# Performance work log

Measured on AMD Instinct MI355X. Metric: run time of the kernel, lower is better.

Reference implementation:

```python
import jax, jax.numpy as jnp
import numpy as np

NUM_ITERATIONS = 5
NUM_TERMS = 3  # (degree + 1) // 2 with degree = 5
INITIAL_SCALE = 1.1


def setup_inputs() -> dict:
    key = jax.random.key(0)
    k1, k2 = jax.random.split(key)
    X = jax.random.normal(k1, (64, 1024, 1024), dtype=jnp.float32)
    coefficients = jnp.array([3.4445, -4.7750, 2.0315], dtype=jnp.float32)
    return {"X": X, "coefficients": coefficients}


def reference(X, coefficients):
    # Normalize each matrix to Frobenius norm INITIAL_SCALE
    fro = jnp.sqrt(jnp.sum(X * X, axis=(-2, -1), keepdims=True))
    X = X / fro * INITIAL_SCALE
    for _ in range(NUM_ITERATIONS):
        # XTX = X^T X, shape [B, M, M]
        XTX = jnp.einsum('bji,bjk->bik', X, X)
        term = X
        acc = coefficients[0] * X
        for i in range(1, NUM_TERMS):
            term = jnp.einsum('bij,bjk->bik', term, XTX)  # X (X^T X)^i
            acc = acc + coefficients[i] * term
        X = acc
    return X
```

## Files before the change

kernel.cpp:

```cpp
#include <hip/hip_runtime.h>
#include <hip/hip_bf16.h>
#include <stdint.h>

typedef float f32x4 __attribute__((ext_vector_type(4)));
typedef short bf16x8 __attribute__((ext_vector_type(8)));

#define LDW 1024
#define BATCH_SH 20

__device__ __forceinline__ float b2f(__hip_bfloat16 h) { return __bfloat162float(h); }
__device__ __forceinline__ __hip_bfloat16 f2b(float f) { return __float2bfloat16(f); }

__device__ __forceinline__ void gload16(const void* g, void* l) {
  __builtin_amdgcn_global_load_lds((const __attribute__((address_space(1))) void*)g,
                                   (__attribute__((address_space(3))) void*)l,
                                   16, 0, 0);
}

__global__ void k_partial(const float* __restrict__ xin, float* __restrict__ partials) {
  const int b = blockIdx.y, ch = blockIdx.x, t = threadIdx.x;
  const size_t base = ((size_t)b << BATCH_SH) + (size_t)ch * 16384;
  float s = 0.f;
#pragma unroll
  for (int i = 0; i < 16; ++i) {
    f32x4 v = *reinterpret_cast<const f32x4*>(xin + base + (size_t)(i * 256 + t) * 4);
    s += v[0] * v[0] + v[1] * v[1] + v[2] * v[2] + v[3] * v[3];
  }
#pragma unroll
  for (int off = 32; off; off >>= 1) s += __shfl_down(s, off);
  __shared__ float red[4];
  if ((t & 63) == 0) red[t >> 6] = s;
  __syncthreads();
  if (t == 0) partials[b * 64 + ch] = red[0] + red[1] + red[2] + red[3];
}

__global__ void k_scalesplit(const float* __restrict__ xin, const float* __restrict__ partials,
                             __hip_bfloat16* __restrict__ Xh, __hip_bfloat16* __restrict__ Xl,
                             __hip_bfloat16* __restrict__ XTh, __hip_bfloat16* __restrict__ XTl) {
  __shared__ float tile[64][65];
  const int b = blockIdx.z, tm = blockIdx.y, tn = blockIdx.x;
  const size_t boff = (size_t)b << BATCH_SH;
  const int t = threadIdx.x, lr0 = t >> 6, lc = t & 63;
  float q = partials[b * 64 + (t & 63)];
#pragma unroll
  for (int off = 32; off; off >>= 1) q += __shfl_down(q, off);
  q = __shfl(q, 0);
  const float s = 1.1f / sqrtf(q);
#pragma unroll
  for (int p = 0; p < 16; ++p) {
    const int lr = p * 4 + lr0;
    const size_t idx = boff + (size_t)(tm * 64 + lr) * LDW + tn * 64 + lc;
    const float v = xin[idx] * s;
    __hip_bfloat16 h = f2b(v);
    Xh[idx] = h;
    Xl[idx] = f2b(v - b2f(h));
    tile[lr][lc] = v;
  }
  __syncthreads();
#pragma unroll
  for (int p = 0; p < 16; ++p) {
    const int lr = p * 4 + lr0;
    const float v = tile[lc][lr];
    const size_t idx = boff + (size_t)(tn * 64 + lr) * LDW + tm * 64 + lc;
    __hip_bfloat16 h = f2b(v);
    XTh[idx] = h;
    XTl[idx] = f2b(v - b2f(h));
  }
}


#define SEGPTRS(S)                                                                        \
  const int seg_ = (S) >> 4, k0_ = ((S) & 15) << 6;                                       \
  const __hip_bfloat16* pa_ = seg_ == 0 ? pa0 : seg_ == 1 ? pa1 : pa2;                    \
  const __hip_bfloat16* pb_ = seg_ == 0 ? pb0 : seg_ == 1 ? pb1 : pb2;

#define STAGE_GL(DB, S)                                                                   \
  {                                                                                       \
    SEGPTRS(S)                                                                            \
    char* lb_ = smem + (DB) * 65536;                                                      \
    _Pragma("unroll") for (int it_ = 0; it_ < 4; ++it_) {                                 \
      const int r_ = it_ * 64 + w * 8 + (l >> 3);                                         \
      const int kx_ = k0_ + (((l & 7) ^ (l >> 3)) << 3);                                  \
      gload16(pa_ + boff + (size_t)(rowA + r_) * LDW + kx_,                               \
              lb_ + (it_ * 64 + w * 8) * 128 + l * 16);                                   \
      gload16(pb_ + boff + (size_t)(rowB + r_) * LDW + kx_,                               \
              lb_ + 32768 + (it_ * 64 + w * 8) * 128 + l * 16);                           \
    }                                                                                     \
  }

#define MFMA_CL(AV, BV)                                                                   \
  __builtin_amdgcn_s_setprio(1);                                                          \
  _Pragma("unroll") for (int mi_ = 0; mi_ < 8; ++mi_)                                     \
      _Pragma("unroll") for (int ni_ = 0; ni_ < 4; ++ni_)                                 \
          acc[mi_][ni_] = __builtin_amdgcn_mfma_f32_16x16x32_bf16(                        \
              AV[mi_], BV[ni_], acc[mi_][ni_], 0, 0, 0);                                  \
  __builtin_amdgcn_s_setprio(0);

#define SCB() __builtin_amdgcn_sched_barrier(0)
#define BAR() __builtin_amdgcn_s_barrier()

template <int MODE>
__global__ __launch_bounds__(512, 2) void k_gemm(
    const __hip_bfloat16* __restrict__ pa0, const __hip_bfloat16* __restrict__ pa1,
    const __hip_bfloat16* __restrict__ pa2, const __hip_bfloat16* __restrict__ pb0,
    const __hip_bfloat16* __restrict__ pb1, const __hip_bfloat16* __restrict__ pb2,
    __hip_bfloat16* oh, __hip_bfloat16* ol,
    __hip_bfloat16* oth, __hip_bfloat16* otl,
    float* __restrict__ of,
    const __hip_bfloat16* __restrict__ eh, const __hip_bfloat16* __restrict__ el,
    const float* __restrict__ coef) {
  __shared__ __align__(16) char smem[131072];
  const int t = threadIdx.x;
  const int w = t >> 6, l = t & 63;
  const int wr = w >> 2, wc = w & 3;

  const int nwg = gridDim.x, q = nwg >> 3, r8 = nwg & 7;
  const int xcd = blockIdx.x & 7, o = blockIdx.x >> 3;
  const int wgid = (xcd < r8 ? xcd * (q + 1) : r8 * (q + 1) + (xcd - r8) * q) + o;

  int bat, tm, tn;
  if constexpr (MODE == 3) {
    bat = wgid >> 4;
    const int tile = wgid & 15;
    tm = tile >> 2; tn = tile & 3;
  } else {
    bat = (int)((unsigned)wgid / 10u);
    const int tile = wgid - bat * 10;
    tm = (tile < 4) ? 0 : (tile < 7) ? 1 : (tile < 9) ? 2 : 3;
    tn = (tile < 4) ? tile : (tile < 7) ? (tile - 3) : (tile < 9) ? (tile - 5) : 3;
  }
  const size_t boff = (size_t)bat << BATCH_SH;
  const int rowA = tm * 256, rowB = tn * 256;

  f32x4 acc[8][4];
#pragma unroll
  for (int i = 0; i < 8; ++i)
#pragma unroll
    for (int j = 0; j < 4; ++j) acc[i][j] = (f32x4){0.f, 0.f, 0.f, 0.f};

  int offA[2][8], offB[2][4];
#pragma unroll
  for (int kk = 0; kk < 2; ++kk) {
    const int g = kk * 4 + (l >> 4);
#pragma unroll
    for (int mi = 0; mi < 8; ++mi) {
      const int rA = wr * 128 + mi * 16 + (l & 15);
      offA[kk][mi] = rA * 128 + ((g ^ (rA & 7)) << 4);
    }
#pragma unroll
    for (int ni = 0; ni < 4; ++ni) {
      const int rB = wc * 64 + ni * 16 + (l & 15);
      offB[kk][ni] = 32768 + rB * 128 + ((g ^ (rB & 7)) << 4);
    }
  }

  STAGE_GL(0, 0);
  STAGE_GL(1, 1);
  asm volatile("s_waitcnt vmcnt(8)" ::: "memory");
  SCB();
  BAR();
  SCB();

  for (int s = 0; s < 48; ++s) {
    const int base = (s & 1) * 65536;
    bf16x8 av0[8], bv0[4], av1[8], bv1[4];
#pragma unroll
    for (int i = 0; i < 8; ++i)
      av0[i] = *reinterpret_cast<const bf16x8*>(smem + base + offA[0][i]);
#pragma unroll
    for (int i = 0; i < 4; ++i)
      bv0[i] = *reinterpret_cast<const bf16x8*>(smem + base + offB[0][i]);
    MFMA_CL(av0, bv0);
#pragma unroll
    for (int i = 0; i < 8; ++i)
      av1[i] = *reinterpret_cast<const bf16x8*>(smem + base + offA[1][i]);
#pragma unroll
    for (int i = 0; i < 4; ++i)
      bv1[i] = *reinterpret_cast<const bf16x8*>(smem + base + offB[1][i]);
    asm volatile("s_waitcnt lgkmcnt(0)" ::: "memory");
    SCB();
    BAR();
    SCB();
    if (s + 2 < 48) STAGE_GL((s & 1), s + 2);
    SCB();
    MFMA_CL(av1, bv1);
    if (s + 2 < 48) {
      asm volatile("s_waitcnt vmcnt(8)" ::: "memory");
    } else {
      asm volatile("s_waitcnt vmcnt(0)" ::: "memory");
    }
    SCB();
    BAR();
    SCB();
  }

  float c0 = 0.f, c1 = 0.f, c2 = 0.f;
  if constexpr (MODE == 2) { c0 = coef[0]; c1 = coef[1]; c2 = coef[2]; }
  const int r0 = tm * 256 + wr * 128 + ((l >> 4) << 2);
  const int cb = tn * 256 + wc * 64 + (l & 15);
#pragma unroll
  for (int mi = 0; mi < 8; ++mi) {
#pragma unroll
    for (int ni = 0; ni < 4; ++ni) {
      const int ccol = cb + ni * 16;
#pragma unroll
      for (int j = 0; j < 4; ++j) {
        const int rrow = r0 + mi * 16 + j;
        const size_t idx = boff + (size_t)rrow * LDW + ccol;
        float v = acc[mi][ni][j];
        if constexpr (MODE == 2)
          v = c2 * v + c1 * (b2f(eh[idx]) + b2f(el[idx])) + (rrow == ccol ? c0 : 0.f);
        __hip_bfloat16 h = f2b(v);
        __hip_bfloat16 lo = f2b(v - b2f(h));
        if constexpr (MODE == 3) {
          if (oh) { oh[idx] = h; ol[idx] = lo; }
          if (of) of[idx] = v;
        } else {
          oh[idx] = h; ol[idx] = lo;
          if (tm != tn) {
            const size_t tix = boff + (size_t)ccol * LDW + rrow;
            oth[tix] = h; otl[tix] = lo;
          }
        }
      }
    }
  }

  if constexpr (MODE == 3) {
    if (oth) {
      unsigned* tlds = reinterpret_cast<unsigned*>(smem);
      unsigned short* pth = reinterpret_cast<unsigned short*>(oth);
      unsigned short* ptl = reinterpret_cast<unsigned short*>(otl);
#pragma unroll
      for (int h2 = 0; h2 < 2; ++h2) {
        __builtin_amdgcn_s_barrier();
        if ((wc >> 1) == h2) {
#pragma unroll
          for (int mi = 0; mi < 8; ++mi) {
#pragma unroll
            for (int ni = 0; ni < 4; ++ni) {
              const int cl = (wc & 1) * 64 + ni * 16 + (l & 15);
#pragma unroll
              for (int j = 0; j < 4; ++j) {
                const int rr = wr * 128 + ((l >> 4) << 2) + mi * 16 + j;
                const float v = acc[mi][ni][j];
                const __hip_bfloat16 hh = f2b(v);
                const __hip_bfloat16 lo = f2b(v - b2f(hh));
                const unsigned pk = (unsigned)(*(const unsigned short*)&hh) |
                                    ((unsigned)(*(const unsigned short*)&lo) << 16);
                tlds[rr * 128 + (cl ^ ((rr >> 1) & 31))] = pk;
              }
            }
          }
        }
        __builtin_amdgcn_s_barrier();
#pragma unroll
        for (int i = 0; i < 16; ++i) {
          const int trow = w * 16 + i;
          const size_t obase =
              boff + (size_t)(tn * 256 + h2 * 128 + trow) * LDW + tm * 256;
#pragma unroll
          for (int c = 0; c < 2; ++c) {
            const int e0 = (c * 64 + l) * 2;
            const int m = (e0 >> 1) & 31;
            const unsigned p0 = tlds[e0 * 128 + (trow ^ m)];
            const unsigned p1 = tlds[(e0 + 1) * 128 + (trow ^ m)];
            *reinterpret_cast<unsigned*>(pth + obase + e0) =
                (p0 & 0xffffu) | (p1 << 16);
            *reinterpret_cast<unsigned*>(ptl + obase + e0) =
                (p0 >> 16) | (p1 & 0xffff0000u);
          }
        }
      }
    }
  }
}

extern "C" void kernel_launch(void* const* d_in, const int* in_sizes, int n_in,
                              void* d_out, int out_size, void* d_ws, size_t ws_size,
                              hipStream_t stream) {
  (void)in_sizes; (void)n_in; (void)out_size;
  const float* xin = (const float*)d_in[0];
  const float* coef = (const float*)d_in[1];
  float* xout = (float*)d_out;

  int CH = 64;
  while (CH > 1 && ((size_t)CH * 16u * 1024u * 1024u + 65536u) > ws_size) CH >>= 1;

  const size_t nE = (size_t)CH << BATCH_SH;
  __hip_bfloat16* P0h = (__hip_bfloat16*)d_ws;
  __hip_bfloat16* P0l = P0h + nE;
  __hip_bfloat16* P1h = P0l + nE;
  __hip_bfloat16* P1l = P1h + nE;
  __hip_bfloat16* P2h = P1l + nE;
  __hip_bfloat16* P2l = P2h + nE;
  __hip_bfloat16* XTh = P2l + nE;
  __hip_bfloat16* XTl = XTh + nE;
  float* partials = (float*)(XTl + nE);

  for (int c = 0; c < 64; c += CH) {
    const float* xi = xin + ((size_t)c << BATCH_SH);
    float* X = xout + ((size_t)c << BATCH_SH);
    k_partial<<<dim3(64, CH), 256, 0, stream>>>(xi, partials);
    k_scalesplit<<<dim3(16, 16, CH), 256, 0, stream>>>(xi, partials, P0h, P0l, XTh, XTl);

    __hip_bfloat16 *Xh = P0h, *Xl = P0l, *Ah = P1h, *Al = P1l, *Bh = P2h, *Bl = P2l;
    for (int it = 0; it < 5; ++it) {
      k_gemm<1><<<dim3(CH * 10), 512, 0, stream>>>(XTh, XTh, XTl, XTh, XTl, XTh,
                                                   Ah, Al, Ah, Al, nullptr,
                                                   nullptr, nullptr, nullptr);
      k_gemm<2><<<dim3(CH * 10), 512, 0, stream>>>(Ah, Ah, Al, Ah, Al, Ah,
                                                   Bh, Bl, Bh, Bl, nullptr,
                                                   Ah, Al, coef);
      k_gemm<3><<<dim3(CH * 16), 512, 0, stream>>>(Xh, Xh, Xl, Bh, Bl, Bh,
                                                   (it < 4) ? Ah : nullptr,
                                                   (it < 4) ? Al : nullptr,
                                                   (it < 4) ? XTh : nullptr,
                                                   (it < 4) ? XTl : nullptr,
                                                   (it == 4) ? X : nullptr,
                                                   nullptr, nullptr, nullptr);
      __hip_bfloat16 *th = Xh, *tl = Xl;
      Xh = Ah; Xl = Al;
      Ah = Bh; Al = Bl;
      Bh = th; Bl = tl;
    }
  }
}
```

Measured before the change: 7.542 ms.

## Restructure GEMM main loop into four-phase LDS/MFMA interleaved pipeline

```diff
diff --git a/kernel.cpp b/kernel.cpp
--- a/kernel.cpp
+++ b/kernel.cpp
@@ -74,11 +74,11 @@
   const __hip_bfloat16* pa_ = seg_ == 0 ? pa0 : seg_ == 1 ? pa1 : pa2;                    \
   const __hip_bfloat16* pb_ = seg_ == 0 ? pb0 : seg_ == 1 ? pb1 : pb2;
 
-#define STAGE_GL(DB, S)                                                                   \
+#define STAGE_GL_H(DB, S, H)                                                              \
   {                                                                                       \
     SEGPTRS(S)                                                                            \
     char* lb_ = smem + (DB) * 65536;                                                      \
-    _Pragma("unroll") for (int it_ = 0; it_ < 4; ++it_) {                                 \
+    _Pragma("unroll") for (int it_ = (H) * 2; it_ < (H) * 2 + 2; ++it_) {                 \
       const int r_ = it_ * 64 + w * 8 + (l >> 3);                                         \
       const int kx_ = k0_ + (((l & 7) ^ (l >> 3)) << 3);                                  \
       gload16(pa_ + boff + (size_t)(rowA + r_) * LDW + kx_,                               \
@@ -88,16 +88,19 @@
     }                                                                                     \
   }
 
-#define MFMA_CL(AV, BV)                                                                   \
+#define STAGE_GL(DB, S) { STAGE_GL_H(DB, S, 0) STAGE_GL_H(DB, S, 1) }
+
+#define MFMA_CL(AV, BV, MH)                                                               \
   __builtin_amdgcn_s_setprio(1);                                                          \
-  _Pragma("unroll") for (int mi_ = 0; mi_ < 8; ++mi_)                                     \
+  _Pragma("unroll") for (int mi_ = 0; mi_ < 4; ++mi_)                                     \
       _Pragma("unroll") for (int ni_ = 0; ni_ < 4; ++ni_)                                 \
-          acc[mi_][ni_] = __builtin_amdgcn_mfma_f32_16x16x32_bf16(                        \
-              AV[mi_], BV[ni_], acc[mi_][ni_], 0, 0, 0);                                  \
+          acc[(MH) * 4 + mi_][ni_] = __builtin_amdgcn_mfma_f32_16x16x32_bf16(             \
+              AV[mi_], BV[ni_], acc[(MH) * 4 + mi_][ni_], 0, 0, 0);                       \
   __builtin_amdgcn_s_setprio(0);
 
 #define SCB() __builtin_amdgcn_sched_barrier(0)
 #define BAR() __builtin_amdgcn_s_barrier()
+#define LDF(P) (*reinterpret_cast<const bf16x8*>(P))
 
 template <int MODE>
 __global__ __launch_bounds__(512, 2) void k_gemm(
@@ -155,43 +158,53 @@
   }
 
   STAGE_GL(0, 0);
-  STAGE_GL(1, 1);
-  asm volatile("s_waitcnt vmcnt(8)" ::: "memory");
+  asm volatile("s_waitcnt vmcnt(0)" ::: "memory");
   SCB();
   BAR();
   SCB();
 
+  bf16x8 avA[4], avB[4], bvA[4], bvB[4];
+#pragma unroll
+  for (int i = 0; i < 4; ++i) avA[i] = LDF(smem + offA[0][i]);
+#pragma unroll
+  for (int i = 0; i < 4; ++i) bvA[i] = LDF(smem + offB[0][i]);
+
   for (int s = 0; s < 48; ++s) {
     const int base = (s & 1) * 65536;
-    bf16x8 av0[8], bv0[4], av1[8], bv1[4];
-#pragma unroll
-    for (int i = 0; i < 8; ++i)
-      av0[i] = *reinterpret_cast<const bf16x8*>(smem + base + offA[0][i]);
-#pragma unroll
-    for (int i = 0; i < 4; ++i)
-      bv0[i] = *reinterpret_cast<const bf16x8*>(smem + base + offB[0][i]);
-    MFMA_CL(av0, bv0);
-#pragma unroll
-    for (int i = 0; i < 8; ++i)
-      av1[i] = *reinterpret_cast<const bf16x8*>(smem + base + offA[1][i]);
-#pragma unroll
-    for (int i = 0; i < 4; ++i)
-      bv1[i] = *reinterpret_cast<const bf16x8*>(smem + base + offB[1][i]);
+    const int nb = ((s & 1) ^ 1) * 65536;
+    const bool pf = (s + 1 < 48);
+    if (pf) STAGE_GL_H((s & 1) ^ 1, s + 1, 0);
+#pragma unroll
+    for (int i = 0; i < 4; ++i) avB[i] = LDF(smem + base + offA[0][4 + i]);
+    SCB();
+    MFMA_CL(avA, bvA, 0);
+    if (pf) STAGE_GL_H((s & 1) ^ 1, s + 1, 1);
+#pragma unroll
+    for (int i = 0; i < 4; ++i) avA[i] = LDF(smem + base + offA[1][i]);
+#pragma unroll
+    for (int i = 0; i < 4; ++i) bvB[i] = LDF(smem + base + offB[1][i]);
+    SCB();
+    MFMA_CL(avB, bvA, 1);
+#pragma unroll
+    for (int i = 0; i < 4; ++i) avB[i] = LDF(smem + base + offA[1][4 + i]);
+    SCB();
+    MFMA_CL(avA, bvB, 0);
     asm volatile("s_waitcnt lgkmcnt(0)" ::: "memory");
     SCB();
+    if (pf) {
+      asm volatile("s_waitcnt vmcnt(0)" ::: "memory");
+      SCB();
+    }
     BAR();
     SCB();
-    if (s + 2 < 48) STAGE_GL((s & 1), s + 2);
-    SCB();
-    MFMA_CL(av1, bv1);
-    if (s + 2 < 48) {
-      asm volatile("s_waitcnt vmcnt(8)" ::: "memory");
-    } else {
-      asm volatile("s_waitcnt vmcnt(0)" ::: "memory");
-    }
-    SCB();
-    BAR();
-    SCB();
+    if (pf) {
+#pragma unroll
+      for (int i = 0; i < 4; ++i) avA[i] = LDF(smem + nb + offA[0][i]);
+#pragma unroll
+      for (int i = 0; i < 4; ++i) bvA[i] = LDF(smem + nb + offB[0][i]);
+    }
+    SCB();
+    MFMA_CL(avB, bvB, 1);
   }
 
   float c0 = 0.f, c1 = 0.f, c2 = 0.f;
```

Result: faster. 7.381 ms (-2.1%).
